# Performance work log

Measured on AMD Instinct MI355X. Metric: run time of the kernel, lower is better.

The kernel has to match this reference:

```python
import jax, jax.numpy as jnp
import numpy as np

# graph sizes: G graphs of N_PER nodes each (block-diagonal batched graph)
G, N_PER, F, NHID, E_PER = 128, 512, 128, 128, 4096
N = G * N_PER
E = G * E_PER
L1, L2, L3 = 4, 2, 2            # PANConv filter sizes (conv1 uses init filter_size=4)
K1, K2, K3 = N_PER // 2, N_PER // 4, N_PER // 8  # ratio=0.5 top-k per pooling stage


def setup_inputs() -> dict:
    ks = jax.random.split(jax.random.key(0), 10)
    rng = np.random.default_rng(0)
    off = (np.arange(G) * N_PER)[:, None]
    src = (rng.integers(0, N_PER, size=(G, E_PER)) + off).reshape(-1)
    dst = (rng.integers(0, N_PER, size=(G, E_PER)) + off).reshape(-1)
    edge_index = jnp.asarray(np.stack([src, dst]).astype(np.int32))
    batch = jnp.repeat(jnp.arange(G, dtype=jnp.int32), N_PER)
    def w(k, shp, fan):
        return jax.random.normal(k, shp, jnp.float32) / np.float32(np.sqrt(fan))
    z = lambda *s: jnp.zeros(s, jnp.float32)
    return dict(
        x=jax.random.normal(ks[0], (N, F), jnp.float32),
        edge_index=edge_index, batch=batch,
        lump_W=w(ks[1], (F, NHID), F), lump_b=z(NHID),
        conv1_W=w(ks[2], (NHID, NHID), NHID), conv1_b=z(NHID),
        conv2_W=w(ks[3], (NHID, NHID), NHID), conv2_b=z(NHID),
        conv3_W=w(ks[4], (NHID, NHID), NHID), conv3_b=z(NHID),
        pool1_p=w(ks[5], (NHID,), NHID), pool1_beta=jnp.full((2,), 0.5, jnp.float32),
        pool2_p=w(ks[6], (NHID,), NHID), pool2_beta=jnp.full((2,), 0.5, jnp.float32),
        pool3_p=w(ks[7], (NHID,), NHID), pool3_beta=jnp.full((2,), 0.5, jnp.float32),
        lin1_W=w(ks[8], (NHID, NHID // 2), NHID), lin1_b=z(NHID // 2),
        lin2_W=w(ks[9], (NHID // 2, 1), NHID // 2), lin2_b=z(1),
    )


def _pan_prop(h, src, dst, ew, L):
    # (sum_{l=0..L} A^l) @ h, A weighted by edge weights ew, via iterated gather/scatter
    acc, y = h, h
    n = h.shape[0]
    for _ in range(L):
        y = jax.ops.segment_sum(y[src] * ew[:, None], dst, num_segments=n)
        acc = acc + y
    return acc


def _pan_conv(x, src, dst, ew, W, b, L):
    # PANConv: M = Z^{-1/2} (sum_{l<=L} A^l) Z^{-1/2};  out = M x W + b
    d = _pan_prop(jnp.ones((x.shape[0], 1), x.dtype), src, dst, ew, L)[:, 0]
    dinv = jax.lax.rsqrt(jnp.maximum(d, 1e-12))
    h = dinv[:, None] * _pan_prop(dinv[:, None] * x, src, dst, ew, L)
    return h @ W + b


def _pan_pool(x, src, dst, ew, p, beta, n_per, k):
    # PANPooling: score = beta0*(x.p)/||p|| + beta1*node_strength; per-graph top-k
    n = x.shape[0]
    deg = jax.ops.segment_sum(ew, dst, num_segments=n)
    score = beta[0] * (x @ p) / jnp.linalg.norm(p) + beta[1] * deg
    _, idx = jax.lax.top_k(score.reshape(G, n_per), k)          # [G, k] local indices
    perm = (idx + (jnp.arange(G) * n_per)[:, None]).reshape(-1)  # [G*k] global
    x_new = x[perm] * jnp.tanh(score[perm])[:, None]
    inv = jnp.zeros((n,), jnp.int32).at[perm].set(jnp.arange(G * k, dtype=jnp.int32))
    mask = jnp.zeros((n,), x.dtype).at[perm].set(1.0)
    # keep edge arrays fixed-size: dropped edges get weight 0 (same math as filtering)
    return x_new, inv[src], inv[dst], ew * mask[src] * mask[dst], perm


def reference(x, edge_index, batch, lump_W, lump_b, conv1_W, conv1_b, conv2_W, conv2_b,
              conv3_W, conv3_b, pool1_p, pool1_beta, pool2_p, pool2_beta, pool3_p,
              pool3_beta, lin1_W, lin1_b, lin2_W, lin2_b):
    src, dst = edge_index[0], edge_index[1]
    ew = jnp.ones((src.shape[0],), x.dtype)
    h = x @ lump_W + lump_b                                   # PANLump lift
    h = _pan_conv(h, src, dst, ew, conv1_W, conv1_b, L1)
    h, src, dst, ew, perm1 = _pan_pool(h, src, dst, ew, pool1_p, pool1_beta, N_PER, K1)
    h = _pan_conv(h, src, dst, ew, conv2_W, conv2_b, L2)
    h, src, dst, ew, perm2 = _pan_pool(h, src, dst, ew, pool2_p, pool2_beta, K1, K2)
    h = _pan_conv(h, src, dst, ew, conv3_W, conv3_b, L3)
    h, src, dst, ew, perm3 = _pan_pool(h, src, dst, ew, pool3_p, pool3_beta, K2, K3)
    seg = jnp.repeat(jnp.arange(G, dtype=jnp.int32), K3)
    mean = jax.ops.segment_sum(h, seg, num_segments=G) / jnp.float32(K3)  # scatter_mean
    out = jax.nn.relu(mean @ lin1_W + lin1_b) @ lin2_W + lin2_b           # [G, 1]
    return out
```

## Files before the change

kernel.cpp:

```cpp
#include <hip/hip_runtime.h>
#include <math.h>

#define G_     128
#define E_     524288
#define EPG    4096
#define DEGMAX 48

typedef __attribute__((ext_vector_type(8))) short bf16x8;
typedef __attribute__((ext_vector_type(4))) float f32x4;
typedef __attribute__((ext_vector_type(4))) unsigned short u16x4;

__device__ inline void split_bf16(float x, short& hi, short& lo){
    unsigned u = __float_as_uint(x);
    hi = (short)(u >> 16);
    float hf = __uint_as_float(u & 0xffff0000u);
    unsigned r = __float_as_uint(x - hf);
    lo = (short)(r >> 16);
}

__global__ __launch_bounds__(256) void k_splitW(const float* __restrict__ W0,
        const float* __restrict__ W1, const float* __restrict__ W2,
        const float* __restrict__ W3, unsigned short* __restrict__ outw){
    int mat = blockIdx.x >> 3, blk = blockIdx.x & 7;
    const float* W = (mat==0)?W0:(mat==1)?W1:(mat==2)?W2:W3;
    unsigned short* hi = outw + (size_t)mat*2*17408;
    unsigned short* lo = hi + 17408;
    for (int e = blk*256 + threadIdx.x; e < 16384; e += 2048){
        int k = e >> 7, n = e & 127;
        short h, l; split_bf16(W[e], h, l);
        hi[n*136 + k] = h; lo[n*136 + k] = l;
    }
}

template<int WAVES>
__device__ void gemm_body(char* smem, int bid, const float* __restrict__ X,
        const unsigned short* __restrict__ Wsp, const float* __restrict__ bias,
        float* __restrict__ Y,
        const float* __restrict__ p, const float* __restrict__ beta,
        const int* __restrict__ cntv, float* __restrict__ score){
    short* wsh = (short*)smem;
    short* wsl = (short*)(smem + 34816);
    float* bsh = (float*)(smem + 69632);
    float* qs  = (float*)(smem + 70144);
    float* rednorm = (float*)(smem + 70656);
    const int NT = WAVES*64;
    int t = threadIdx.x;
    {
        const unsigned* h32 = (const unsigned*)Wsp;
        const unsigned* l32 = (const unsigned*)(Wsp + 17408);
        unsigned* wsh32 = (unsigned*)wsh;
        unsigned* wsl32 = (unsigned*)wsl;
        for (int i = t; i < 8704; i += NT){ wsh32[i] = h32[i]; wsl32[i] = l32[i]; }
    }
    if (t < 128) bsh[t] = bias[t];
    if (score && t < 64){ float a = p[t], b = p[t+64]; rednorm[t] = a*a + b*b; }
    __syncthreads();
    float b1 = 0.f;
    if (score){
        if (t == 0){ float s = 0.f; for (int i = 0; i < 64; i++) s += rednorm[i]; rednorm[0] = sqrtf(s); }
        __syncthreads();
        if (t < 128) qs[t] = beta[0] * p[t] / rednorm[0];
        b1 = beta[1];
        __syncthreads();
    }
    int wave = t >> 6, lane = t & 63;
    int ln = lane & 15, q = lane >> 4;
    size_t rb = (size_t)bid * (WAVES*16);
    const float* xrow = &X[(rb + wave*16 + ln)*128 + q*8];
    f32x4 acc[8];
    #pragma unroll
    for (int i = 0; i < 8; i++) acc[i] = (f32x4){0.f,0.f,0.f,0.f};
    #pragma unroll
    for (int kc = 0; kc < 4; kc++){
        float4 xa = *(const float4*)(xrow + kc*32);
        float4 xb = *(const float4*)(xrow + kc*32 + 4);
        bf16x8 ah, al; short hi, lo;
        split_bf16(xa.x, hi, lo); ah[0]=hi; al[0]=lo;
        split_bf16(xa.y, hi, lo); ah[1]=hi; al[1]=lo;
        split_bf16(xa.z, hi, lo); ah[2]=hi; al[2]=lo;
        split_bf16(xa.w, hi, lo); ah[3]=hi; al[3]=lo;
        split_bf16(xb.x, hi, lo); ah[4]=hi; al[4]=lo;
        split_bf16(xb.y, hi, lo); ah[5]=hi; al[5]=lo;
        split_bf16(xb.z, hi, lo); ah[6]=hi; al[6]=lo;
        split_bf16(xb.w, hi, lo); ah[7]=hi; al[7]=lo;
        #pragma unroll
        for (int nt = 0; nt < 8; nt++){
            int wo = (nt*16 + ln)*136 + kc*32 + q*8;
            bf16x8 bh = *(const bf16x8*)&wsh[wo];
            bf16x8 bl = *(const bf16x8*)&wsl[wo];
            acc[nt] = __builtin_amdgcn_mfma_f32_16x16x32_bf16(ah, bh, acc[nt], 0, 0, 0);
            acc[nt] = __builtin_amdgcn_mfma_f32_16x16x32_bf16(ah, bl, acc[nt], 0, 0, 0);
            acc[nt] = __builtin_amdgcn_mfma_f32_16x16x32_bf16(al, bh, acc[nt], 0, 0, 0);
        }
    }
    #pragma unroll
    for (int nt = 0; nt < 8; nt++){
        int c = nt*16 + ln;
        float bb = bsh[c];
        #pragma unroll
        for (int r = 0; r < 4; r++){
            Y[(rb + wave*16 + q*4 + r)*128 + c] = acc[nt][r] + bb;
        }
    }
    if (score){
        #pragma unroll
        for (int r = 0; r < 4; r++){
            float sp = 0.f;
            #pragma unroll
            for (int nt = 0; nt < 8; nt++){
                int c = nt*16 + ln;
                sp += (acc[nt][r] + bsh[c]) * qs[c];
            }
            sp += __shfl_xor(sp, 1);
            sp += __shfl_xor(sp, 2);
            sp += __shfl_xor(sp, 4);
            sp += __shfl_xor(sp, 8);
            if (ln == 0){
                int row = (int)rb + wave*16 + q*4 + r;
                score[row] = sp + b1 * (float)cntv[row];
            }
        }
    }
}

template<int WAVES>
__global__ __launch_bounds__(WAVES*64) void k_gemm_mfma(const float* __restrict__ X,
        const unsigned short* __restrict__ Wsp, const float* __restrict__ bias,
        float* __restrict__ Y,
        const float* __restrict__ p, const float* __restrict__ beta,
        const int* __restrict__ cntv, float* __restrict__ score){
    __shared__ __align__(16) char smem[70912];
    gemm_body<WAVES>(smem, blockIdx.x, X, Wsp, bias, Y, p, beta, cntv, score);
}

__global__ __launch_bounds__(512) void k_prep1(const int* __restrict__ ei,
        int* __restrict__ cnt, unsigned short* __restrict__ csrcp,
        int* __restrict__ permg, float* __restrict__ dinvg){
    __shared__ int   lcnt[512];
    __shared__ __align__(16) unsigned short csrS[512*DEGMAX + 8];
    __shared__ float y[1024];
    __shared__ int   bins[64];
    __shared__ int   permS[512];
    int g = blockIdx.x, t = threadIdx.x, gbase = g*512;
    lcnt[t] = 0;
    if (t < 64) bins[t] = 0;
    unsigned* c32 = (unsigned*)csrS;
    for (int i = t; i < 512*DEGMAX/2 + 4; i += 512) c32[i] = 0;
    __syncthreads();
    for (int i = t; i < EPG; i += 512){
        int e = g*EPG + i;
        int sv = ei[e] & 511;
        int d  = ei[E_ + e] & 511;
        int slot = atomicAdd(&lcnt[d], 1);
        if (slot < DEGMAX) csrS[d*DEGMAX + slot] = (unsigned short)sv;
    }
    __syncthreads();
    {
        unsigned* dst = (unsigned*)(csrcp + (size_t)gbase*DEGMAX);
        for (int i = t; i < 512*DEGMAX/2; i += 512) dst[i] = c32[i];
    }
    int rawc = lcnt[t];
    cnt[gbase + t] = rawc;
    int dc = min(rawc, DEGMAX);
    atomicAdd(&bins[dc], 1);
    __syncthreads();
    if (t < 64){
        int v0 = bins[t], s = v0;
        #pragma unroll
        for (int off = 1; off < 64; off <<= 1){
            int n = __shfl_up(s, off);
            if (t >= off) s += n;
        }
        bins[t] = s - v0;
    }
    __syncthreads();
    {
        int slot = atomicAdd(&bins[dc], 1);
        int pk = t | (dc << 16);
        permS[slot] = pk;
        permg[gbase + slot] = pk;
    }
    __syncthreads();
    int pk = permS[t];
    int pv = pk & 0xffff, pd = pk >> 16;
    y[pv] = 1.f;
    __syncthreads();
    float dacc = 1.f;
    int cur = 0;
    for (int l = 0; l < 4; l++){
        const float* la = &y[cur*512];
        float s = 0.f;
        int nq = (pd + 3) >> 2;
        const u16x4* cp = (const u16x4*)(csrS + pv*DEGMAX);
        u16x4 oc = cp[0];
        #pragma unroll 1
        for (int jq = 0; jq < nq; jq++){
            u16x4 ocn = cp[jq + 1];
            s += (la[(int)oc[0]] + la[(int)oc[1]]) + (la[(int)oc[2]] + la[(int)oc[3]]);
            oc = ocn;
        }
        if (nq) s -= (float)(nq*4 - pd) * la[0];
        y[(1^cur)*512 + pv] = s;
        dacc += s;
        __syncthreads();
        cur ^= 1;
    }
    dinvg[gbase + pv] = rsqrtf(fmaxf(dacc, 1e-12f));
}

template<int NPER, int L, int IT, bool SEL>
__global__ __launch_bounds__(1024)
void k_prop(const int* __restrict__ permg, const float* __restrict__ dinvg,
        const unsigned short* __restrict__ csrcp,
        const float* __restrict__ X, const int* __restrict__ selg,
        const float* __restrict__ thg, float* __restrict__ OUT){
    __shared__ __align__(16) float y[NPER*32];
    __shared__ float dinvs[NPER];
    int g = blockIdx.x, fq = blockIdx.y, gbase = g*NPER;
    int t = threadIdx.x;
    int f4 = (t & 7)*4;
    int fo = fq*32 + f4;
    if (t < NPER) dinvs[t] = dinvg[gbase + t];
    int pkr[IT];
    {
        int wv = t >> 6, gi = (t >> 3) & 7;
        #pragma unroll
        for (int it = 0; it < IT; it++){
            int ch = (it & 1) ? (15 - wv) : wv;
            pkr[it] = permg[gbase + (16*it + ch)*8 + gi];
        }
    }
    __syncthreads();
    float4 acc[IT];
    #pragma unroll
    for (int it = 0; it < IT; it++){
        int v = pkr[it] & 0xffff;
        float d = dinvs[v];
        size_t row;
        if (SEL){
            row = (size_t)selg[gbase + v];
            d *= thg[gbase + v];
        } else {
            row = (size_t)(gbase + v);
        }
        float4 w = *(const float4*)&X[row*128 + fo];
        w.x*=d; w.y*=d; w.z*=d; w.w*=d;
        acc[it] = w;
        *(float4*)&y[v*32 + f4] = w;
    }
    __syncthreads();
    for (int l = 0; l < L; l++){
        float4 s[IT];
        #pragma unroll
        for (int it = 0; it < IT; it++){
            int pk = pkr[it];
            int c = pk >> 16;
            int nq = (c + 3) >> 2;
            const u16x4* cp = (const u16x4*)(csrcp + (size_t)(gbase + (pk & 0xffff))*DEGMAX);
            float4 ss = make_float4(0.f,0.f,0.f,0.f);
            u16x4 oc = cp[0];
            #pragma unroll 1
            for (int jq = 0; jq < nq; jq++){
                u16x4 ocn = cp[jq + 1];
                float4 w0 = *(const float4*)&y[((int)oc[0])*32 + f4];
                float4 w1 = *(const float4*)&y[((int)oc[1])*32 + f4];
                float4 w2 = *(const float4*)&y[((int)oc[2])*32 + f4];
                float4 w3 = *(const float4*)&y[((int)oc[3])*32 + f4];
                ss.x += (w0.x + w1.x) + (w2.x + w3.x);
                ss.y += (w0.y + w1.y) + (w2.y + w3.y);
                ss.z += (w0.z + w1.z) + (w2.z + w3.z);
                ss.w += (w0.w + w1.w) + (w2.w + w3.w);
                oc = ocn;
            }
            if (nq){
                float fp = (float)(nq*4 - c);
                float4 z = *(const float4*)&y[f4];
                ss.x -= fp*z.x; ss.y -= fp*z.y; ss.z -= fp*z.z; ss.w -= fp*z.w;
            }
            s[it] = ss;
        }
        __syncthreads();
        #pragma unroll
        for (int it = 0; it < IT; it++){
            int v = pkr[it] & 0xffff;
            *(float4*)&y[v*32 + f4] = s[it];
            acc[it].x+=s[it].x; acc[it].y+=s[it].y; acc[it].z+=s[it].z; acc[it].w+=s[it].w;
        }
        __syncthreads();
    }
    #pragma unroll
    for (int it = 0; it < IT; it++){
        int v = pkr[it] & 0xffff;
        float d = dinvs[v];
        float4 w = acc[it];
        w.x*=d; w.y*=d; w.z*=d; w.w*=d;
        *(float4*)&OUT[(size_t)(gbase + v)*128 + fo] = w;
    }
}

template<int NPER, bool BUILD>
__global__ __launch_bounds__(512) void k_pooltop(const float* __restrict__ score_in,
        const int* __restrict__ esrc_in, const int* __restrict__ edst_in,
        int* __restrict__ esrc_out, int* __restrict__ edst_out,
        int* __restrict__ cnt_next, unsigned short* __restrict__ csrcp,
        int* __restrict__ permg, float* __restrict__ dinvg,
        int* __restrict__ selg, float* __restrict__ thg){
    const int K = NPER/2;
    constexpr int CSRSZ = BUILD ? (NPER/2)*DEGMAX + 8 : 8;
    __shared__ __align__(16) float sc[NPER];
    __shared__ int  nid[NPER];
    __shared__ int  lcnt[NPER/2];
    __shared__ int  bins[64];
    __shared__ int  permS[NPER/2];
    __shared__ __align__(16) unsigned short csrS[CSRSZ];
    int g = blockIdx.x, t = threadIdx.x, gbase = g*NPER;
    if (t < K) lcnt[t] = 0;
    if (t < 64) bins[t] = 0;
    if (BUILD){
        unsigned* c32 = (unsigned*)csrS;
        for (int i = t; i < K*DEGMAX/2 + 4; i += 512) c32[i] = 0;
    }
    if (t < NPER) sc[t] = score_in[gbase + t];
    __syncthreads();
    if (t < NPER){
        float s = sc[t];
        int rank = 0;
        const float4* sc4 = (const float4*)sc;
        #pragma unroll 8
        for (int j4 = 0; j4 < NPER/4; j4++){
            float4 v = sc4[j4];
            int j = j4*4;
            rank += (v.x > s) || (v.x == s && (j+0) < t);
            rank += (v.y > s) || (v.y == s && (j+1) < t);
            rank += (v.z > s) || (v.z == s && (j+2) < t);
            rank += (v.w > s) || (v.w == s && (j+3) < t);
        }
        if (rank < K){
            nid[t] = g*K + rank;
            selg[g*K + rank] = gbase + t;
            thg[g*K + rank]  = tanhf(s);
        } else nid[t] = -1;
    }
    __syncthreads();
    if (BUILD){
        for (int i = t; i < EPG; i += 512){
            int e = g*EPG + i;
            int d = edst_in[e];
            if (d < 0) continue;
            int s_ = esrc_in[e];
            int ns = nid[s_ - gbase], nd = nid[d - gbase];
            if ((ns | nd) < 0){ edst_out[e] = -1; }
            else {
                esrc_out[e] = ns; edst_out[e] = nd;
                int ndl = nd & (K-1);
                int slot = atomicAdd(&lcnt[ndl], 1);
                if (slot < DEGMAX) csrS[ndl*DEGMAX + slot] = (unsigned short)(ns & (K-1));
            }
        }
        __syncthreads();
        {
            unsigned* c32 = (unsigned*)csrS;
            unsigned* dst = (unsigned*)(csrcp + (size_t)g*K*DEGMAX);
            for (int i = t; i < K*DEGMAX/2; i += 512) dst[i] = c32[i];
        }
        float* yd = sc;
        int rawc = 0, dc = 0;
        if (t < K){
            rawc = lcnt[t];
            cnt_next[g*K + t] = rawc;
            dc = min(rawc, DEGMAX);
            atomicAdd(&bins[dc], 1);
        }
        __syncthreads();
        if (t < 64){
            int v0 = bins[t], s = v0;
            #pragma unroll
            for (int off = 1; off < 64; off <<= 1){
                int n = __shfl_up(s, off);
                if (t >= off) s += n;
            }
            bins[t] = s - v0;
        }
        __syncthreads();
        if (t < K){
            int slot = atomicAdd(&bins[dc], 1);
            permS[slot] = t | (dc << 16);
            permg[g*K + slot] = permS[slot];
        }
        __syncthreads();
        int pv = 0, pd = 0;
        if (t < K){
            int pk = permS[t];
            pv = pk & 0xffff; pd = pk >> 16;
            yd[pv] = 1.f;
        }
        __syncthreads();
        float dacc = 1.f;
        int cur = 0;
        for (int l = 0; l < 2; l++){
            if (t < K){
                const float* la = &yd[cur*K];
                float s = 0.f;
                int nq = (pd + 3) >> 2;
                const u16x4* cp = (const u16x4*)(csrS + pv*DEGMAX);
                u16x4 oc = cp[0];
                #pragma unroll 1
                for (int jq = 0; jq < nq; jq++){
                    u16x4 ocn = cp[jq + 1];
                    s += (la[(int)oc[0]] + la[(int)oc[1]]) + (la[(int)oc[2]] + la[(int)oc[3]]);
                    oc = ocn;
                }
                if (nq) s -= (float)(nq*4 - pd) * la[0];
                yd[(1^cur)*K + pv] = s;
                dacc += s;
            }
            __syncthreads();
            cur ^= 1;
        }
        if (t < K) dinvg[g*K + pv] = rsqrtf(fmaxf(dacc, 1e-12f));
    }
}

__global__ __launch_bounds__(512) void k_stage3(const float* __restrict__ X,
        const unsigned short* __restrict__ Wsp, const float* __restrict__ bias,
        const float* __restrict__ p, const float* __restrict__ beta,
        const int* __restrict__ cntv,
        const float* __restrict__ W1, const float* __restrict__ b1,
        const float* __restrict__ W2, const float* __restrict__ b2,
        float* __restrict__ out){
    __shared__ __align__(16) char smem[70912];
    __shared__ float scs[128];
    __shared__ float thS[64];
    __shared__ int   selS[64];
    __shared__ float mr[128];
    short* wsh = (short*)smem;
    short* wsl = (short*)(smem + 34816);
    float* bsh = (float*)(smem + 69632);
    float* qs  = (float*)(smem + 70144);
    float* rednorm = (float*)(smem + 70656);
    int g = blockIdx.x, t = threadIdx.x;
    {
        const unsigned* h32 = (const unsigned*)Wsp;
        const unsigned* l32 = (const unsigned*)(Wsp + 17408);
        unsigned* wsh32 = (unsigned*)wsh;
        unsigned* wsl32 = (unsigned*)wsl;
        for (int i = t; i < 8704; i += 512){ wsh32[i] = h32[i]; wsl32[i] = l32[i]; }
    }
    if (t < 128) bsh[t] = bias[t];
    if (t < 64){ float a = p[t], b = p[t+64]; rednorm[t] = a*a + b*b; }
    __syncthreads();
    if (t == 0){ float s = 0.f; for (int i = 0; i < 64; i++) s += rednorm[i]; rednorm[0] = sqrtf(s); }
    __syncthreads();
    if (t < 128) qs[t] = beta[0] * p[t] / rednorm[0];
    float b1v = beta[1];
    __syncthreads();
    int wave = t >> 6, lane = t & 63;
    int ln = lane & 15, q = lane >> 4;
    const float* xrow = &X[((size_t)g*128 + wave*16 + ln)*128 + q*8];
    f32x4 acc[8];
    #pragma unroll
    for (int i = 0; i < 8; i++) acc[i] = (f32x4){0.f,0.f,0.f,0.f};
    #pragma unroll
    for (int kc = 0; kc < 4; kc++){
        float4 xa = *(const float4*)(xrow + kc*32);
        float4 xb = *(const float4*)(xrow + kc*32 + 4);
        bf16x8 ah, al; short hi, lo;
        split_bf16(xa.x, hi, lo); ah[0]=hi; al[0]=lo;
        split_bf16(xa.y, hi, lo); ah[1]=hi; al[1]=lo;
        split_bf16(xa.z, hi, lo); ah[2]=hi; al[2]=lo;
        split_bf16(xa.w, hi, lo); ah[3]=hi; al[3]=lo;
        split_bf16(xb.x, hi, lo); ah[4]=hi; al[4]=lo;
        split_bf16(xb.y, hi, lo); ah[5]=hi; al[5]=lo;
        split_bf16(xb.z, hi, lo); ah[6]=hi; al[6]=lo;
        split_bf16(xb.w, hi, lo); ah[7]=hi; al[7]=lo;
        #pragma unroll
        for (int nt = 0; nt < 8; nt++){
            int wo = (nt*16 + ln)*136 + kc*32 + q*8;
            bf16x8 bh = *(const bf16x8*)&wsh[wo];
            bf16x8 bl = *(const bf16x8*)&wsl[wo];
            acc[nt] = __builtin_amdgcn_mfma_f32_16x16x32_bf16(ah, bh, acc[nt], 0, 0, 0);
            acc[nt] = __builtin_amdgcn_mfma_f32_16x16x32_bf16(ah, bl, acc[nt], 0, 0, 0);
            acc[nt] = __builtin_amdgcn_mfma_f32_16x16x32_bf16(al, bh, acc[nt], 0, 0, 0);
        }
    }
    #pragma unroll
    for (int r = 0; r < 4; r++){
        float sp = 0.f;
        #pragma unroll
        for (int nt = 0; nt < 8; nt++){
            int c = nt*16 + ln;
            sp += (acc[nt][r] + bsh[c]) * qs[c];
        }
        sp += __shfl_xor(sp, 1);
        sp += __shfl_xor(sp, 2);
        sp += __shfl_xor(sp, 4);
        sp += __shfl_xor(sp, 8);
        if (ln == 0){
            int rl = wave*16 + q*4 + r;
            scs[rl] = sp + b1v * (float)cntv[g*128 + rl];
        }
    }
    __syncthreads();
    float* Yl = (float*)smem;
    #pragma unroll
    for (int nt = 0; nt < 8; nt++){
        int c = nt*16 + ln;
        float bb = bsh[c];
        #pragma unroll
        for (int r = 0; r < 4; r++){
            Yl[(wave*16 + q*4 + r)*132 + c] = acc[nt][r] + bb;
        }
    }
    __syncthreads();
    if (t < 128){
        float s = scs[t];
        int rank = 0;
        const float4* sc4 = (const float4*)scs;
        #pragma unroll 8
        for (int j4 = 0; j4 < 32; j4++){
            float4 v = sc4[j4];
            int j = j4*4;
            rank += (v.x > s) || (v.x == s && (j+0) < t);
            rank += (v.y > s) || (v.y == s && (j+1) < t);
            rank += (v.z > s) || (v.z == s && (j+2) < t);
            rank += (v.w > s) || (v.w == s && (j+3) < t);
        }
        if (rank < 64){ selS[rank] = t; thS[rank] = tanhf(s); }
    }
    __syncthreads();
    if (t < 128){
        float s = 0.f;
        #pragma unroll 8
        for (int r = 0; r < 64; r++) s += Yl[selS[r]*132 + t] * thS[r];
        mr[t] = s * (1.f/64.f);
    }
    __syncthreads();
    if (t < 64){
        float a = b1[t];
        #pragma unroll 8
        for (int k = 0; k < 128; k++) a += mr[k]*W1[k*64 + t];
        a = fmaxf(a, 0.f);
        float r = a * W2[t];
        #pragma unroll
        for (int off = 32; off > 0; off >>= 1) r += __shfl_down(r, off);
        if (t == 0) out[g] = r + b2[0];
    }
}

extern "C" void kernel_launch(void* const* d_in, const int* in_sizes, int n_in,
                              void* d_out, int out_size, void* d_ws, size_t ws_size,
                              hipStream_t stream){
    (void)in_sizes; (void)n_in; (void)out_size; (void)ws_size;
    const float* x     = (const float*)d_in[0];
    const int*   ei    = (const int*)d_in[1];
    const float* lumpW = (const float*)d_in[3];
    const float* lumpb = (const float*)d_in[4];
    const float* convW[3]    = {(const float*)d_in[5], (const float*)d_in[7], (const float*)d_in[9]};
    const float* convB[3]    = {(const float*)d_in[6], (const float*)d_in[8], (const float*)d_in[10]};
    const float* poolP[3]    = {(const float*)d_in[11], (const float*)d_in[13], (const float*)d_in[15]};
    const float* poolBeta[3] = {(const float*)d_in[12], (const float*)d_in[14], (const float*)d_in[16]};
    const float* lin1W = (const float*)d_in[17];
    const float* lin1b = (const float*)d_in[18];
    const float* lin2W = (const float*)d_in[19];
    const float* lin2b = (const float*)d_in[20];
    float* out = (float*)d_out;

    char* w8 = (char*)d_ws;
    size_t off = 0;
    auto alloc = [&](size_t bytes)->char*{
        char* p = w8 + off; off += (bytes + 255) & ~(size_t)255; return p;
    };
    float* A     = (float*)alloc((size_t)65536*128*4);
    float* Bb    = (float*)alloc((size_t)65536*128*4);
    int*   srcA  = (int*)alloc((size_t)E_*4);
    int*   dstA  = (int*)alloc((size_t)E_*4);
    unsigned short* csr1 = (unsigned short*)alloc((size_t)65536*DEGMAX*2);
    unsigned short* csr2 = (unsigned short*)alloc((size_t)32768*DEGMAX*2);
    unsigned short* csr3 = (unsigned short*)alloc((size_t)16384*DEGMAX*2);
    int*   cntA  = (int*)alloc((size_t)(65536+32768+16384)*4);
    int*   cnt1 = cntA, *cnt2 = cntA + 65536, *cnt3 = cntA + 98304;
    int*   perm1 = (int*)alloc((size_t)65536*4);
    int*   perm2 = (int*)alloc((size_t)32768*4);
    int*   perm3 = (int*)alloc((size_t)16384*4);
    float* dinv1 = (float*)alloc((size_t)65536*4);
    float* dinv2 = (float*)alloc((size_t)32768*4);
    float* dinv3 = (float*)alloc((size_t)16384*4);
    float* score1 = (float*)alloc((size_t)65536*4);
    float* score2 = (float*)alloc((size_t)32768*4);
    int*   sel2  = (int*)alloc((size_t)32768*4);
    int*   sel3  = (int*)alloc((size_t)16384*4);
    float* th2   = (float*)alloc((size_t)32768*4);
    float* th3   = (float*)alloc((size_t)16384*4);
    unsigned short* wsp = (unsigned short*)alloc((size_t)4*2*17408*2);
    unsigned short* wspLump = wsp;
    unsigned short* wspC0   = wsp + 1*2*17408;
    unsigned short* wspC1   = wsp + 2*2*17408;
    unsigned short* wspC2   = wsp + 3*2*17408;

    k_splitW<<<32, 256, 0, stream>>>(lumpW, convW[0], convW[1], convW[2], wsp);
    k_prep1<<<G_, 512, 0, stream>>>(ei, cnt1, csr1, perm1, dinv1);
    k_gemm_mfma<8><<<512, 512, 0, stream>>>(x, wspLump, lumpb, A,
            nullptr, nullptr, nullptr, nullptr);

    k_prop<512,4,4,false><<<dim3(G_,4), 1024, 0, stream>>>(perm1, dinv1, csr1, A,
            nullptr, nullptr, Bb);
    k_gemm_mfma<8><<<512, 512, 0, stream>>>(Bb, wspC0, convB[0], A,
            poolP[0], poolBeta[0], cnt1, score1);
    k_pooltop<512,true><<<G_, 512, 0, stream>>>(score1, ei, ei + E_, srcA, dstA,
            cnt2, csr2, perm2, dinv2, sel2, th2);

    k_prop<256,2,2,true><<<dim3(G_,4), 1024, 0, stream>>>(perm2, dinv2, csr2, A,
            sel2, th2, Bb);
    k_gemm_mfma<8><<<256, 512, 0, stream>>>(Bb, wspC1, convB[1], A,
            poolP[1], poolBeta[1], cnt2, score2);
    k_pooltop<256,true><<<G_, 512, 0, stream>>>(score2, srcA, dstA, srcA, dstA,
            cnt3, csr3, perm3, dinv3, sel3, th3);

    k_prop<128,2,1,true><<<dim3(G_,4), 1024, 0, stream>>>(perm3, dinv3, csr3, A,
            sel3, th3, Bb);
    k_stage3<<<G_, 512, 0, stream>>>(Bb, wspC2, convB[2],
            poolP[2], poolBeta[2], cnt3, lin1W, lin1b, lin2W, lin2b, out);
}
```

Measured before the change: 273.9 us.

## Fuse graph prep, lump GEMM and weight splitting into one launch

Merges three independent startup kernels (CSR/degree prep for stage 1, the lump linear GEMM, and the bf16 hi/lo splitting of the conv weights) into one heterogeneous launch that dispatches on block index. The lump GEMM now splits its fp32 weights into shared memory directly instead of reading a pre-split buffer. The aim is to cut two kernel launches and their serialization gaps and let the independent work overlap on the GPU. In exchange, every GEMM block redoes the lump weight split, and all blocks share the larger shared-memory footprint. k_pooltop loses its BUILD template flag, since both call sites already used true.

```diff
diff --git a/kernel.cpp b/kernel.cpp
--- a/kernel.cpp
+++ b/kernel.cpp
@@ -18,24 +18,10 @@
     lo = (short)(r >> 16);
 }
 
-__global__ __launch_bounds__(256) void k_splitW(const float* __restrict__ W0,
-        const float* __restrict__ W1, const float* __restrict__ W2,
-        const float* __restrict__ W3, unsigned short* __restrict__ outw){
-    int mat = blockIdx.x >> 3, blk = blockIdx.x & 7;
-    const float* W = (mat==0)?W0:(mat==1)?W1:(mat==2)?W2:W3;
-    unsigned short* hi = outw + (size_t)mat*2*17408;
-    unsigned short* lo = hi + 17408;
-    for (int e = blk*256 + threadIdx.x; e < 16384; e += 2048){
-        int k = e >> 7, n = e & 127;
-        short h, l; split_bf16(W[e], h, l);
-        hi[n*136 + k] = h; lo[n*136 + k] = l;
-    }
-}
-
 template<int WAVES>
 __device__ void gemm_body(char* smem, int bid, const float* __restrict__ X,
-        const unsigned short* __restrict__ Wsp, const float* __restrict__ bias,
-        float* __restrict__ Y,
+        const unsigned short* __restrict__ Wsp, const float* __restrict__ Wf,
+        const float* __restrict__ bias, float* __restrict__ Y,
         const float* __restrict__ p, const float* __restrict__ beta,
         const int* __restrict__ cntv, float* __restrict__ score){
     short* wsh = (short*)smem;
@@ -45,12 +31,18 @@
     float* rednorm = (float*)(smem + 70656);
     const int NT = WAVES*64;
     int t = threadIdx.x;
-    {
+    if (Wsp){
         const unsigned* h32 = (const unsigned*)Wsp;
         const unsigned* l32 = (const unsigned*)(Wsp + 17408);
         unsigned* wsh32 = (unsigned*)wsh;
         unsigned* wsl32 = (unsigned*)wsl;
         for (int i = t; i < 8704; i += NT){ wsh32[i] = h32[i]; wsl32[i] = l32[i]; }
+    } else {
+        for (int e = t; e < 16384; e += NT){
+            int k = e >> 7, n = e & 127;
+            short hi, lo; split_bf16(Wf[e], hi, lo);
+            wsh[n*136 + k] = hi; wsl[n*136 + k] = lo;
+        }
     }
     if (t < 128) bsh[t] = bias[t];
     if (score && t < 64){ float a = p[t], b = p[t+64]; rednorm[t] = a*a + b*b; }
@@ -123,25 +115,15 @@
     }
 }
 
-template<int WAVES>
-__global__ __launch_bounds__(WAVES*64) void k_gemm_mfma(const float* __restrict__ X,
-        const unsigned short* __restrict__ Wsp, const float* __restrict__ bias,
-        float* __restrict__ Y,
-        const float* __restrict__ p, const float* __restrict__ beta,
-        const int* __restrict__ cntv, float* __restrict__ score){
-    __shared__ __align__(16) char smem[70912];
-    gemm_body<WAVES>(smem, blockIdx.x, X, Wsp, bias, Y, p, beta, cntv, score);
-}
-
-__global__ __launch_bounds__(512) void k_prep1(const int* __restrict__ ei,
+__device__ void prep1_body(char* smem, int g, const int* __restrict__ ei,
         int* __restrict__ cnt, unsigned short* __restrict__ csrcp,
         int* __restrict__ permg, float* __restrict__ dinvg){
-    __shared__ int   lcnt[512];
-    __shared__ __align__(16) unsigned short csrS[512*DEGMAX + 8];
-    __shared__ float y[1024];
-    __shared__ int   bins[64];
-    __shared__ int   permS[512];
-    int g = blockIdx.x, t = threadIdx.x, gbase = g*512;
+    int*   lcnt  = (int*)smem;
+    unsigned short* csrS = (unsigned short*)(smem + 2048);
+    float* y     = (float*)(smem + 51216);
+    int*   bins  = (int*)(smem + 55312);
+    int*   permS = (int*)(smem + 55568);
+    int t = threadIdx.x, gbase = g*512;
     lcnt[t] = 0;
     if (t < 64) bins[t] = 0;
     unsigned* c32 = (unsigned*)csrS;
@@ -206,6 +188,164 @@
         cur ^= 1;
     }
     dinvg[gbase + pv] = rsqrtf(fmaxf(dacc, 1e-12f));
+}
+
+__global__ __launch_bounds__(512) void k_fused0(const int* __restrict__ ei,
+        int* __restrict__ cnt1, unsigned short* __restrict__ csr1,
+        int* __restrict__ perm1, float* __restrict__ dinv1,
+        const float* __restrict__ x, const float* __restrict__ lumpW,
+        const float* __restrict__ lumpb, float* __restrict__ A,
+        const float* __restrict__ cw0, const float* __restrict__ cw1,
+        const float* __restrict__ cw2, unsigned short* __restrict__ wsp){
+    __shared__ __align__(16) char smem[70912];
+    int bid = blockIdx.x;
+    if (bid < G_){
+        prep1_body(smem, bid, ei, cnt1, csr1, perm1, dinv1);
+    } else if (bid < G_ + 512){
+        gemm_body<8>(smem, bid - G_, x, nullptr, lumpW, lumpb, A,
+                     nullptr, nullptr, nullptr, nullptr);
+    } else {
+        int idx = bid - (G_ + 512);
+        int mat = idx >> 3, blk = idx & 7;
+        const float* W = (mat==0)?cw0:(mat==1)?cw1:cw2;
+        unsigned short* hi = wsp + (size_t)mat*2*17408;
+        unsigned short* lo = hi + 17408;
+        for (int e = blk*512 + threadIdx.x; e < 16384; e += 4096){
+            int k = e >> 7, n = e & 127;
+            short h, l; split_bf16(W[e], h, l);
+            hi[n*136 + k] = h; lo[n*136 + k] = l;
+        }
+    }
+}
+
+template<int WAVES>
+__global__ __launch_bounds__(WAVES*64) void k_gemm_mfma(const float* __restrict__ X,
+        const unsigned short* __restrict__ Wsp, const float* __restrict__ bias,
+        float* __restrict__ Y,
+        const float* __restrict__ p, const float* __restrict__ beta,
+        const int* __restrict__ cntv, float* __restrict__ score){
+    __shared__ __align__(16) char smem[70912];
+    gemm_body<WAVES>(smem, blockIdx.x, X, Wsp, nullptr, bias, Y, p, beta, cntv, score);
+}
+
+template<int NPER>
+__global__ __launch_bounds__(512) void k_pooltop(const float* __restrict__ score_in,
+        const int* __restrict__ esrc_in, const int* __restrict__ edst_in,
+        int* __restrict__ esrc_out, int* __restrict__ edst_out,
+        int* __restrict__ cnt_next, unsigned short* __restrict__ csrcp,
+        int* __restrict__ permg, float* __restrict__ dinvg,
+        int* __restrict__ selg, float* __restrict__ thg){
+    const int K = NPER/2;
+    __shared__ __align__(16) float sc[NPER];
+    __shared__ int  nid[NPER];
+    __shared__ int  lcnt[NPER/2];
+    __shared__ int  bins[64];
+    __shared__ int  permS[NPER/2];
+    __shared__ __align__(16) unsigned short csrS[(NPER/2)*DEGMAX + 8];
+    int g = blockIdx.x, t = threadIdx.x, gbase = g*NPER;
+    if (t < K) lcnt[t] = 0;
+    if (t < 64) bins[t] = 0;
+    {
+        unsigned* c32 = (unsigned*)csrS;
+        for (int i = t; i < K*DEGMAX/2 + 4; i += 512) c32[i] = 0;
+    }
+    if (t < NPER) sc[t] = score_in[gbase + t];
+    __syncthreads();
+    if (t < NPER){
+        float s = sc[t];
+        int rank = 0;
+        const float4* sc4 = (const float4*)sc;
+        #pragma unroll 8
+        for (int j4 = 0; j4 < NPER/4; j4++){
+            float4 v = sc4[j4];
+            int j = j4*4;
+            rank += (v.x > s) || (v.x == s && (j+0) < t);
+            rank += (v.y > s) || (v.y == s && (j+1) < t);
+            rank += (v.z > s) || (v.z == s && (j+2) < t);
+            rank += (v.w > s) || (v.w == s && (j+3) < t);
+        }
+        if (rank < K){
+            nid[t] = g*K + rank;
+            selg[g*K + rank] = gbase + t;
+            thg[g*K + rank]  = tanhf(s);
+        } else nid[t] = -1;
+    }
+    __syncthreads();
+    for (int i = t; i < EPG; i += 512){
+        int e = g*EPG + i;
+        int d = edst_in[e];
+        if (d < 0) continue;
+        int s_ = esrc_in[e];
+        int ns = nid[s_ - gbase], nd = nid[d - gbase];
+        if ((ns | nd) < 0){ edst_out[e] = -1; }
+        else {
+            esrc_out[e] = ns; edst_out[e] = nd;
+            int ndl = nd & (K-1);
+            int slot = atomicAdd(&lcnt[ndl], 1);
+            if (slot < DEGMAX) csrS[ndl*DEGMAX + slot] = (unsigned short)(ns & (K-1));
+        }
+    }
+    __syncthreads();
+    {
+        unsigned* c32 = (unsigned*)csrS;
+        unsigned* dst = (unsigned*)(csrcp + (size_t)g*K*DEGMAX);
+        for (int i = t; i < K*DEGMAX/2; i += 512) dst[i] = c32[i];
+    }
+    float* yd = sc;
+    int rawc = 0, dc = 0;
+    if (t < K){
+        rawc = lcnt[t];
+        cnt_next[g*K + t] = rawc;
+        dc = min(rawc, DEGMAX);
+        atomicAdd(&bins[dc], 1);
+    }
+    __syncthreads();
+    if (t < 64){
+        int v0 = bins[t], s = v0;
+        #pragma unroll
+        for (int off = 1; off < 64; off <<= 1){
+            int n = __shfl_up(s, off);
+            if (t >= off) s += n;
+        }
+        bins[t] = s - v0;
+    }
+    __syncthreads();
+    int pv = 0, pd = 0;
+    if (t < K){
+        int slot = atomicAdd(&bins[dc], 1);
+        permS[slot] = t | (dc << 16);
+        permg[g*K + slot] = permS[slot];
+    }
+    __syncthreads();
+    if (t < K){
+        int pk = permS[t];
+        pv = pk & 0xffff; pd = pk >> 16;
+        yd[pv] = 1.f;
+    }
+    __syncthreads();
+    float dacc = 1.f;
+    int cur = 0;
+    for (int l = 0; l < 2; l++){
+        if (t < K){
+            const float* la = &yd[cur*K];
+            float s = 0.f;
+            int nq = (pd + 3) >> 2;
+            const u16x4* cp = (const u16x4*)(csrS + pv*DEGMAX);
+            u16x4 oc = cp[0];
+            #pragma unroll 1
+            for (int jq = 0; jq < nq; jq++){
+                u16x4 ocn = cp[jq + 1];
+                s += (la[(int)oc[0]] + la[(int)oc[1]]) + (la[(int)oc[2]] + la[(int)oc[3]]);
+                oc = ocn;
+            }
+            if (nq) s -= (float)(nq*4 - pd) * la[0];
+            yd[(1^cur)*K + pv] = s;
+            dacc += s;
+        }
+        __syncthreads();
+        cur ^= 1;
+    }
+    if (t < K) dinvg[g*K + pv] = rsqrtf(fmaxf(dacc, 1e-12f));
 }
 
 template<int NPER, int L, int IT, bool SEL>
@@ -298,129 +438,6 @@
     }
 }
 
-template<int NPER, bool BUILD>
-__global__ __launch_bounds__(512) void k_pooltop(const float* __restrict__ score_in,
-        const int* __restrict__ esrc_in, const int* __restrict__ edst_in,
-        int* __restrict__ esrc_out, int* __restrict__ edst_out,
-        int* __restrict__ cnt_next, unsigned short* __restrict__ csrcp,
-        int* __restrict__ permg, float* __restrict__ dinvg,
-        int* __restrict__ selg, float* __restrict__ thg){
-    const int K = NPER/2;
-    constexpr int CSRSZ = BUILD ? (NPER/2)*DEGMAX + 8 : 8;
-    __shared__ __align__(16) float sc[NPER];
-    __shared__ int  nid[NPER];
-    __shared__ int  lcnt[NPER/2];
-    __shared__ int  bins[64];
-    __shared__ int  permS[NPER/2];
-    __shared__ __align__(16) unsigned short csrS[CSRSZ];
-    int g = blockIdx.x, t = threadIdx.x, gbase = g*NPER;
-    if (t < K) lcnt[t] = 0;
-    if (t < 64) bins[t] = 0;
-    if (BUILD){
-        unsigned* c32 = (unsigned*)csrS;
-        for (int i = t; i < K*DEGMAX/2 + 4; i += 512) c32[i] = 0;
-    }
-    if (t < NPER) sc[t] = score_in[gbase + t];
-    __syncthreads();
-    if (t < NPER){
-        float s = sc[t];
-        int rank = 0;
-        const float4* sc4 = (const float4*)sc;
-        #pragma unroll 8
-        for (int j4 = 0; j4 < NPER/4; j4++){
-            float4 v = sc4[j4];
-            int j = j4*4;
-            rank += (v.x > s) || (v.x == s && (j+0) < t);
-            rank += (v.y > s) || (v.y == s && (j+1) < t);
-            rank += (v.z > s) || (v.z == s && (j+2) < t);
-            rank += (v.w > s) || (v.w == s && (j+3) < t);
-        }
-        if (rank < K){
-            nid[t] = g*K + rank;
-            selg[g*K + rank] = gbase + t;
-            thg[g*K + rank]  = tanhf(s);
-        } else nid[t] = -1;
-    }
-    __syncthreads();
-    if (BUILD){
-        for (int i = t; i < EPG; i += 512){
-            int e = g*EPG + i;
-            int d = edst_in[e];
-            if (d < 0) continue;
-            int s_ = esrc_in[e];
-            int ns = nid[s_ - gbase], nd = nid[d - gbase];
-            if ((ns | nd) < 0){ edst_out[e] = -1; }
-            else {
-                esrc_out[e] = ns; edst_out[e] = nd;
-                int ndl = nd & (K-1);
-                int slot = atomicAdd(&lcnt[ndl], 1);
-                if (slot < DEGMAX) csrS[ndl*DEGMAX + slot] = (unsigned short)(ns & (K-1));
-            }
-        }
-        __syncthreads();
-        {
-            unsigned* c32 = (unsigned*)csrS;
-            unsigned* dst = (unsigned*)(csrcp + (size_t)g*K*DEGMAX);
-            for (int i = t; i < K*DEGMAX/2; i += 512) dst[i] = c32[i];
-        }
-        float* yd = sc;
-        int rawc = 0, dc = 0;
-        if (t < K){
-            rawc = lcnt[t];
-            cnt_next[g*K + t] = rawc;
-            dc = min(rawc, DEGMAX);
-            atomicAdd(&bins[dc], 1);
-        }
-        __syncthreads();
-        if (t < 64){
-            int v0 = bins[t], s = v0;
-            #pragma unroll
-            for (int off = 1; off < 64; off <<= 1){
-                int n = __shfl_up(s, off);
-                if (t >= off) s += n;
-            }
-            bins[t] = s - v0;
-        }
-        __syncthreads();
-        if (t < K){
-            int slot = atomicAdd(&bins[dc], 1);
-            permS[slot] = t | (dc << 16);
-            permg[g*K + slot] = permS[slot];
-        }
-        __syncthreads();
-        int pv = 0, pd = 0;
-        if (t < K){
-            int pk = permS[t];
-            pv = pk & 0xffff; pd = pk >> 16;
-            yd[pv] = 1.f;
-        }
-        __syncthreads();
-        float dacc = 1.f;
-        int cur = 0;
-        for (int l = 0; l < 2; l++){
-            if (t < K){
-                const float* la = &yd[cur*K];
-                float s = 0.f;
-                int nq = (pd + 3) >> 2;
-                const u16x4* cp = (const u16x4*)(csrS + pv*DEGMAX);
-                u16x4 oc = cp[0];
-                #pragma unroll 1
-                for (int jq = 0; jq < nq; jq++){
-                    u16x4 ocn = cp[jq + 1];
-                    s += (la[(int)oc[0]] + la[(int)oc[1]]) + (la[(int)oc[2]] + la[(int)oc[3]]);
-                    oc = ocn;
-                }
-                if (nq) s -= (float)(nq*4 - pd) * la[0];
-                yd[(1^cur)*K + pv] = s;
-                dacc += s;
-            }
-            __syncthreads();
-            cur ^= 1;
-        }
-        if (t < K) dinvg[g*K + pv] = rsqrtf(fmaxf(dacc, 1e-12f));
-    }
-}
-
 __global__ __launch_bounds__(512) void k_stage3(const float* __restrict__ X,
         const unsigned short* __restrict__ Wsp, const float* __restrict__ bias,
         const float* __restrict__ p, const float* __restrict__ beta,
@@ -591,29 +608,26 @@
     int*   sel3  = (int*)alloc((size_t)16384*4);
     float* th2   = (float*)alloc((size_t)32768*4);
     float* th3   = (float*)alloc((size_t)16384*4);
-    unsigned short* wsp = (unsigned short*)alloc((size_t)4*2*17408*2);
-    unsigned short* wspLump = wsp;
-    unsigned short* wspC0   = wsp + 1*2*17408;
-    unsigned short* wspC1   = wsp + 2*2*17408;
-    unsigned short* wspC2   = wsp + 3*2*17408;
-
-    k_splitW<<<32, 256, 0, stream>>>(lumpW, convW[0], convW[1], convW[2], wsp);
-    k_prep1<<<G_, 512, 0, stream>>>(ei, cnt1, csr1, perm1, dinv1);
-    k_gemm_mfma<8><<<512, 512, 0, stream>>>(x, wspLump, lumpb, A,
-            nullptr, nullptr, nullptr, nullptr);
+    unsigned short* wsp = (unsigned short*)alloc((size_t)3*2*17408*2);
+    unsigned short* wspC0 = wsp;
+    unsigned short* wspC1 = wsp + 1*2*17408;
+    unsigned short* wspC2 = wsp + 2*2*17408;
+
+    k_fused0<<<G_ + 512 + 24, 512, 0, stream>>>(ei, cnt1, csr1, perm1, dinv1,
+            x, lumpW, lumpb, A, convW[0], convW[1], convW[2], wsp);
 
     k_prop<512,4,4,false><<<dim3(G_,4), 1024, 0, stream>>>(perm1, dinv1, csr1, A,
             nullptr, nullptr, Bb);
     k_gemm_mfma<8><<<512, 512, 0, stream>>>(Bb, wspC0, convB[0], A,
             poolP[0], poolBeta[0], cnt1, score1);
-    k_pooltop<512,true><<<G_, 512, 0, stream>>>(score1, ei, ei + E_, srcA, dstA,
+    k_pooltop<512><<<G_, 512, 0, stream>>>(score1, ei, ei + E_, srcA, dstA,
             cnt2, csr2, perm2, dinv2, sel2, th2);
 
     k_prop<256,2,2,true><<<dim3(G_,4), 1024, 0, stream>>>(perm2, dinv2, csr2, A,
             sel2, th2, Bb);
     k_gemm_mfma<8><<<256, 512, 0, stream>>>(Bb, wspC1, convB[1], A,
             poolP[1], poolBeta[1], cnt2, score2);
-    k_pooltop<256,true><<<G_, 512, 0, stream>>>(score2, srcA, dstA, srcA, dstA,
+    k_pooltop<256><<<G_, 512, 0, stream>>>(score2, srcA, dstA, srcA, dstA,
             cnt3, csr3, perm3, dinv3, sel3, th3);
 
     k_prop<128,2,1,true><<<dim3(G_,4), 1024, 0, stream>>>(perm3, dinv3, csr3, A,
```

After: 286.4 us. +4.6%, slower.
